# Kernel optimization log

Hardware: AMD Instinct MI355X
Metric: run time of the kernel (lower is better)

## Reference

```python
import jax, jax.numpy as jnp
import numpy as np

B, S, L, D = 128, 256, 200, 768
POS_VOCAB, POS_DIM = 60, 50
REDUC, HID, TAGS, POL = 400, 150, 5, 4


def setup_inputs() -> dict:
    key = jax.random.key(0)
    ks = jax.random.split(key, 12)
    bert_vectors = jax.random.normal(ks[0], (B, S, D), dtype=jnp.float32)
    # ragged subword spans: word j covers subwords [start_j, end_j] (inclusive), length 1..3,
    # skipping the [CLS] token at index 0. Clipped to S-1 (long sentences just truncate).
    rng = np.random.default_rng(0)
    lens = rng.integers(1, 4, size=(B, L))
    cum = np.cumsum(lens, axis=1)
    starts = 1 + cum - lens
    ends = cum
    starts = np.minimum(starts, S - 1)
    ends = np.minimum(ends, S - 1)
    ends = np.maximum(ends, starts)
    positions = jnp.asarray(np.stack([starts, ends], axis=-1), dtype=jnp.int32)
    postag = jax.random.randint(ks[1], (B, L), 1, POS_VOCAB).astype(jnp.int32)

    def lin(k, o, i):
        return jax.random.normal(k, (o, i), jnp.float32) / np.float32(np.sqrt(i))

    return dict(
        bert_vectors=bert_vectors,
        positions=positions,
        postag=postag,
        embed_table=jax.random.normal(ks[2], (POS_VOCAB, POS_DIM), jnp.float32) * 0.02,
        W_reduc=lin(ks[3], REDUC, D + POS_DIM), b_reduc=jnp.zeros((REDUC,), jnp.float32),
        W_ap=lin(ks[4], HID, REDUC), b_ap=jnp.zeros((HID,), jnp.float32),
        W_op=lin(ks[5], HID, REDUC), b_op=jnp.zeros((HID,), jnp.float32),
        W_ap2=lin(ks[6], HID, REDUC), b_ap2=jnp.zeros((HID,), jnp.float32),
        W_op2=lin(ks[7], HID, REDUC), b_op2=jnp.zeros((HID,), jnp.float32),
        W_aptag=lin(ks[8], TAGS, HID), b_aptag=jnp.zeros((TAGS,), jnp.float32),
        W_optag=lin(ks[9], TAGS, HID), b_optag=jnp.zeros((TAGS,), jnp.float32),
        W_bi=lin(ks[10], POL * HID, HID + 1),
    )


def _pool_subwords(vectors, positions):
    # variable-length mean pooling of subword vectors into word vectors
    # vectors: [B,S,D], positions: [B,L,2] -> [B,L,D]
    idx = jnp.arange(S)[None, None, :]                      # [1,1,S]
    p0 = positions[..., 0][..., None]                       # [B,L,1]
    p1 = positions[..., 1][..., None]
    m = ((idx >= p0) & (idx <= p1)).astype(vectors.dtype)   # [B,L,S]
    cnt = jnp.maximum(m.sum(-1, keepdims=True), 1.0)
    return jnp.einsum('bls,bsd->bld', m, vectors) / cnt


def reference(bert_vectors, positions, postag, embed_table,
              W_reduc, b_reduc, W_ap, b_ap, W_op, b_op,
              W_ap2, b_ap2, W_op2, b_op2,
              W_aptag, b_aptag, W_optag, b_optag, W_bi):
    word_vecs = _pool_subwords(bert_vectors, positions)                 # [B,L,D]
    pos_emb = embed_table[postag]                                       # [B,L,50]
    h = jnp.concatenate([pos_emb, word_vecs], axis=-1)                  # [B,L,D+50]
    reduc = jnp.einsum('blf,of->blo', h, W_reduc) + b_reduc             # [B,L,400]
    ap_rep = jax.nn.relu(jnp.einsum('blf,of->blo', reduc, W_ap) + b_ap)
    op_rep = jax.nn.relu(jnp.einsum('blf,of->blo', reduc, W_op) + b_op)
    ap_node = jax.nn.relu(jnp.einsum('blf,of->blo', reduc, W_ap2) + b_ap2)
    op_node = jax.nn.relu(jnp.einsum('blf,of->blo', reduc, W_op2) + b_op2)
    ap_out = jnp.einsum('blf,of->blo', ap_rep, W_aptag) + b_aptag       # [B,L,5]
    op_out = jnp.einsum('blf,of->blo', op_rep, W_optag) + b_optag       # [B,L,5]
    # Biaffine(150,150,POL,bias=(True,False))
    ones = jnp.ones((B, L, 1), ap_node.dtype)
    in1 = jnp.concatenate([ap_node, ones], axis=-1)                     # [B,L,151]
    affine = jnp.einsum('bli,oi->blo', in1, W_bi).reshape(B, L * POL, HID)
    tri = jnp.einsum('bkh,bmh->bkm', affine, op_node)                   # [B,L*POL,L]
    triplet_out = tri.transpose(0, 2, 1).reshape(B, L, L, POL)          # [B,L2,L1,POL]
    return (ap_out, op_out, triplet_out)
```

## Files before the change

kernel.cpp:

```cpp
#include <hip/hip_runtime.h>
#include <hip/hip_bf16.h>

#define Bsz 128
#define Ssz 256
#define Lsz 200
#define Dsz 768
#define POS_DIM 50
#define TAGS 5
#define NROW 25600
#define FIN 818
#define KH 832
#define KD 160
#define KW 416

typedef __attribute__((ext_vector_type(8))) short short8;
typedef __attribute__((ext_vector_type(4))) short short4v;
typedef __attribute__((ext_vector_type(4))) float floatx4;

__device__ __forceinline__ short f2bf(float v) {
    __hip_bfloat16 h = __float2bfloat16(v);
    short s; __builtin_memcpy(&s, &h, 2); return s;
}
__device__ __forceinline__ float bf2f(short s) {
    __hip_bfloat16 h; __builtin_memcpy(&h, &s, 2);
    return __bfloat162float(h);
}

__device__ __forceinline__ void gload16(const short* g, short* l) {
    __builtin_amdgcn_global_load_lds(
        (const __attribute__((address_space(1))) void*)g,
        (__attribute__((address_space(3))) void*)l, 16, 0, 0);
}

__global__ void prep_kernel(const float* __restrict__ W_reduc,
                            const float* __restrict__ W_ap, const float* __restrict__ W_op,
                            const float* __restrict__ W_ap2, const float* __restrict__ W_op2,
                            const float* __restrict__ W_bi,
                            const float* __restrict__ b_reduc,
                            const float* __restrict__ b_ap, const float* __restrict__ b_op,
                            const float* __restrict__ b_ap2, const float* __restrict__ b_op2,
                            short* __restrict__ Wh_bf, short* __restrict__ WrT_bf,
                            short* __restrict__ Wbi_bf,
                            float* __restrict__ b2, float* __restrict__ bbi_pad)
{
    int i = blockIdx.x * blockDim.x + threadIdx.x;
    if (i < 640 * KW) {
        int r = i / KW, c = i % KW;
        float v = 0.0f;
        if (r < 600 && c < 400) {
            const float* src = (r < 150) ? W_ap : (r < 300) ? W_op : (r < 450) ? W_ap2 : W_op2;
            v = src[(r % 150) * 400 + c];
        }
        Wh_bf[i] = f2bf(v);
    }
    if (i < 896 * KW) {
        int k = i / KW, c = i % KW;
        float v = 0.0f;
        if (c < 400) {
            int sc = -1;
            if (k < 768)      sc = POS_DIM + k;
            else if (k < 818) sc = k - 768;
            if (sc >= 0) v = W_reduc[c * FIN + sc];
        }
        WrT_bf[i] = f2bf(v);
    }
    if (i < 640 * KD) {
        int r = i / KD, c = i % KD;
        Wbi_bf[i] = (r < 600 && c < 150) ? f2bf(W_bi[r * 151 + c]) : (short)0;
    }
    if (i < 640) {
        float v = 0.0f;
        if (i < 600) {
            const float* bs = (i < 150) ? b_ap : (i < 300) ? b_op : (i < 450) ? b_ap2 : b_op2;
            v = bs[i % 150];
            const float* wsrc = (i < 150) ? W_ap : (i < 300) ? W_op : (i < 450) ? W_ap2 : W_op2;
            const float* wrow = wsrc + (i % 150) * 400;
            float d = 0.0f;
            for (int c = 0; c < 400; ++c) d += wrow[c] * b_reduc[c];
            v += d;
        }
        b2[i] = v;
        bbi_pad[i] = (i < 600) ? W_bi[i * 151 + 150] : 0.0f;
    }
}

__global__ __launch_bounds__(256) void pool_kernel(
    const float* __restrict__ bert,
    const int* __restrict__ positions,
    const int* __restrict__ postag,
    const float* __restrict__ embed,
    short* __restrict__ h_bf)
{
    int row = blockIdx.x;
    int b = row / Lsz;
    int st = positions[row * 2 + 0];
    int en = positions[row * 2 + 1];
    int tag = postag[row];
    int span = en - st + 1;
    float inv = 1.0f / (float)span;
    const float* base = bert + ((long)b * Ssz + st) * Dsz;
    short* hr = h_bf + (long)row * KH;

    int t = threadIdx.x;
    int c0 = t * 4;
    if (c0 >= KH) return;
    short4v o;
    if (c0 < 768) {
        float4 s = {0.f, 0.f, 0.f, 0.f};
        for (int i = 0; i < span; ++i) {
            float4 v = *(const float4*)(base + i * Dsz + c0);
            s.x += v.x; s.y += v.y; s.z += v.z; s.w += v.w;
        }
        o.x = f2bf(s.x * inv); o.y = f2bf(s.y * inv);
        o.z = f2bf(s.z * inv); o.w = f2bf(s.w * inv);
    } else {
        const float* e = embed + tag * POS_DIM;
#pragma unroll
        for (int j = 0; j < 4; ++j) {
            int c = c0 + j - 768;
            float v = (c < POS_DIM) ? e[c] : 0.0f;
            ((short*)&o)[j] = f2bf(v);
        }
    }
    *(short4v*)(hr + c0) = o;
}

__global__ __launch_bounds__(256) void gemm_mfma(
    const short* __restrict__ A, long long sAb, int lda,
    const short* __restrict__ Bt, long long sBb, int ldb,
    const float* __restrict__ bias,
    short* __restrict__ outB, float* __restrict__ outF, long long sCb, int ldc,
    int M, int Nv, int K, int mode)
{
    __shared__ __align__(16) short AB[16384];

    int bz = blockIdx.z;
    A += (long long)bz * sAb;
    Bt += (long long)bz * sBb;

    int bx = blockIdx.x, by = blockIdx.y;
    if (gridDim.z == 1) {
        int nwg = gridDim.x * gridDim.y;
        int orig = by * gridDim.x + bx;
        int q = nwg >> 3, r = nwg & 7;
        int xcd = orig & 7, idx = orig >> 3;
        int swz = (xcd < r ? xcd * (q + 1) : r * (q + 1) + (xcd - r) * q) + idx;
        bx = swz % gridDim.x;
        by = swz / gridDim.x;
    }

    int row0 = by * 128;
    int col0 = bx * 128;
    int tid = threadIdx.x;
    int lane = tid & 63;
    int wv = tid >> 6;
    int lm = lane & 15, lk = lane >> 4;
    int wr = (wv >> 1) * 64;
    int wc = (wv & 1) * 64;

    int c0 = tid, c1 = tid + 256;
    const short* gA0 = A + (long)(row0 + (c0 & 127)) * lda + (c0 >> 7) * 8;
    const short* gA1 = A + (long)(row0 + (c1 & 127)) * lda + (c1 >> 7) * 8;
    const short* gB0 = Bt + (long)(col0 + (c0 & 127)) * ldb + (c0 >> 7) * 8;
    const short* gB1 = Bt + (long)(col0 + (c1 & 127)) * ldb + (c1 >> 7) * 8;

    floatx4 acc[4][4];
#pragma unroll
    for (int i = 0; i < 4; ++i)
#pragma unroll
        for (int j = 0; j < 4; ++j)
            acc[i][j] = (floatx4){0.f, 0.f, 0.f, 0.f};

    auto stage = [&](int buf, int koff) {
        short* base = &AB[buf * 8192];
        gload16(gA0 + koff, base + c0 * 8);
        gload16(gA1 + koff, base + c1 * 8);
        gload16(gB0 + koff, base + 4096 + c0 * 8);
        gload16(gB1 + koff, base + 4096 + c1 * 8);
    };
    auto compute = [&](int buf) {
        const short* fa = &AB[buf * 8192 + (lk * 128 + wr + lm) * 8];
        const short* fb = &AB[buf * 8192 + 4096 + (lk * 128 + wc + lm) * 8];
        short8 a[4], b[4];
#pragma unroll
        for (int mt = 0; mt < 4; ++mt) a[mt] = *(const short8*)(fa + mt * 128);
#pragma unroll
        for (int nt = 0; nt < 4; ++nt) b[nt] = *(const short8*)(fb + nt * 128);
#pragma unroll
        for (int mt = 0; mt < 4; ++mt)
#pragma unroll
            for (int nt = 0; nt < 4; ++nt)
                acc[mt][nt] = __builtin_amdgcn_mfma_f32_16x16x32_bf16(
                    a[mt], b[nt], acc[mt][nt], 0, 0, 0);
    };

    int nt = K >> 5;
    stage(0, 0);
    __syncthreads();
    int cur = 0;
    for (int t = 0; t + 1 < nt; ++t) {
        stage(cur ^ 1, (t + 1) << 5);
        compute(cur);
        __syncthreads();
        cur ^= 1;
    }
    compute(cur);

#pragma unroll
    for (int mt = 0; mt < 4; ++mt) {
#pragma unroll
        for (int nt = 0; nt < 4; ++nt) {
#pragma unroll
            for (int r = 0; r < 4; ++r) {
                int gm = row0 + wr + mt * 16 + lk * 4 + r;
                int gn = col0 + wc + nt * 16 + lm;
                float v = acc[mt][nt][r];
                if (mode == 0 || mode == 4) {
                    if (gn < Nv)
                        outB[(long)gm * ldc + gn] = f2bf(mode == 0 ? v + bias[gn] : v);
                } else if (mode == 1) {
                    if (gn < 600) {
                        v = fmaxf(v + bias[gn], 0.0f);
                        outB[((long)(gn / 150) * NROW + gm) * KD + gn % 150] = f2bf(v);
                    } else if (gn < 640) {
                        int q = gn - 600;
                        outB[((long)(q / 10) * NROW + gm) * KD + 150 + q % 10] = 0;
                    }
                } else if (mode == 2) {
                    int bb = gm / 200, l = gm % 200;
                    if (gn < 600) {
                        v += bias[gn];
                        outB[((long)bb * 800 + l * 4 + gn / 150) * KD + gn % 150] = f2bf(v);
                    } else if (gn < 640) {
                        int q = gn - 600;
                        outB[((long)bb * 800 + l * 4 + q / 10) * KD + 150 + q % 10] = 0;
                    }
                } else {
                    if (gm < M && gn < Nv)
                        outF[(long long)bz * sCb + (long)gm * ldc + gn] = v;
                }
            }
        }
    }
}

__global__ __launch_bounds__(256) void gemm_mfma64(
    const short* __restrict__ A, int lda,
    const short* __restrict__ Bt, int ldb,
    const float* __restrict__ bias,
    short* __restrict__ outB, int K)
{
    __shared__ __align__(16) short AB[24576];

    int bx = blockIdx.x, by = blockIdx.y;
    {
        int nwg = gridDim.x * gridDim.y;
        int orig = by * gridDim.x + bx;
        int q = nwg >> 3, r = nwg & 7;
        int xcd = orig & 7, idx = orig >> 3;
        int swz = (xcd < r ? xcd * (q + 1) : r * (q + 1) + (xcd - r) * q) + idx;
        bx = swz % gridDim.x;
        by = swz / gridDim.x;
    }

    int row0 = by * 64;
    int col0 = bx * 128;
    int tid = threadIdx.x;
    int lane = tid & 63;
    int wv = tid >> 6;
    int lm = lane & 15, lk = lane >> 4;

    int a0 = tid, a1 = tid + 256;
    const short* gA0 = A + (long)(row0 + (a0 & 63)) * lda + (a0 >> 6) * 8;
    const short* gA1 = A + (long)(row0 + (a1 & 63)) * lda + (a1 >> 6) * 8;
    const short* gB[4];
    int bc[4];
#pragma unroll
    for (int i = 0; i < 4; ++i) {
        bc[i] = tid + i * 256;
        gB[i] = Bt + (long)(col0 + (bc[i] & 127)) * ldb + (bc[i] >> 7) * 8;
    }

    floatx4 acc[4][2];
#pragma unroll
    for (int i = 0; i < 4; ++i)
#pragma unroll
        for (int j = 0; j < 2; ++j)
            acc[i][j] = (floatx4){0.f, 0.f, 0.f, 0.f};

    auto stage = [&](int buf, int koff) {
        short* base = &AB[buf * 12288];
        gload16(gA0 + koff, base + a0 * 8);
        gload16(gA1 + koff, base + a1 * 8);
#pragma unroll
        for (int i = 0; i < 4; ++i)
            gload16(gB[i] + koff, base + 4096 + bc[i] * 8);
    };
    auto compute = [&](int buf) {
        const short* base = &AB[buf * 12288];
#pragma unroll
        for (int kk = 0; kk < 2; ++kk) {
            const short* fa = base + ((kk * 4 + lk) * 64 + lm) * 8;
            const short* fb = base + 4096 + ((kk * 4 + lk) * 128 + wv * 32 + lm) * 8;
            short8 a[4], b[2];
#pragma unroll
            for (int mt = 0; mt < 4; ++mt) a[mt] = *(const short8*)(fa + mt * 128);
#pragma unroll
            for (int nt = 0; nt < 2; ++nt) b[nt] = *(const short8*)(fb + nt * 128);
#pragma unroll
            for (int mt = 0; mt < 4; ++mt)
#pragma unroll
                for (int nt = 0; nt < 2; ++nt)
                    acc[mt][nt] = __builtin_amdgcn_mfma_f32_16x16x32_bf16(
                        a[mt], b[nt], acc[mt][nt], 0, 0, 0);
        }
    };

    int nt = K >> 6;
    stage(0, 0);
    __syncthreads();
    int cur = 0;
    for (int t = 0; t + 1 < nt; ++t) {
        stage(cur ^ 1, (t + 1) << 6);
        compute(cur);
        __syncthreads();
        cur ^= 1;
    }
    compute(cur);

#pragma unroll
    for (int mt = 0; mt < 4; ++mt) {
#pragma unroll
        for (int nt = 0; nt < 2; ++nt) {
#pragma unroll
            for (int r = 0; r < 4; ++r) {
                int gm = row0 + mt * 16 + lk * 4 + r;
                int gn = col0 + wv * 32 + nt * 16 + lm;
                float v = acc[mt][nt][r];
                if (gn < 600) {
                    v = fmaxf(v + bias[gn], 0.0f);
                    outB[((long)(gn / 150) * NROW + gm) * KD + gn % 150] = f2bf(v);
                } else if (gn < 640) {
                    int q = gn - 600;
                    outB[((long)(q / 10) * NROW + gm) * KD + 150 + q % 10] = 0;
                }
            }
        }
    }
}

__global__ __launch_bounds__(256) void tags_kernel(
    const short* __restrict__ hid4,
    const float* __restrict__ W_aptag, const float* __restrict__ b_aptag,
    const float* __restrict__ W_optag, const float* __restrict__ b_optag,
    float* __restrict__ out_ap, float* __restrict__ out_op)
{
    int wave = threadIdx.x / 64;
    int lane = threadIdx.x % 64;
    int row = blockIdx.x * 4 + wave;
    if (row >= NROW) return;

#pragma unroll
    for (int which = 0; which < 2; ++which) {
        const short* rep = hid4 + ((long)which * NROW + row) * KD;
        const float* W = which ? W_optag : W_aptag;
        const float* bb = which ? b_optag : b_aptag;
        float* out = which ? out_op : out_ap;
        float v0 = bf2f(rep[lane]);
        float v1 = bf2f(rep[64 + lane]);
        float v2 = (lane < 22) ? bf2f(rep[128 + lane]) : 0.0f;
#pragma unroll
        for (int t = 0; t < TAGS; ++t) {
            const float* w = W + t * 150;
            float p = v0 * w[lane] + v1 * w[64 + lane] +
                      ((lane < 22) ? v2 * w[128 + lane] : 0.0f);
#pragma unroll
            for (int off = 32; off > 0; off >>= 1) p += __shfl_down(p, off);
            if (lane == 0) out[row * TAGS + t] = p + bb[t];
        }
    }
}

extern "C" void kernel_launch(void* const* d_in, const int* in_sizes, int n_in,
                              void* d_out, int out_size, void* d_ws, size_t ws_size,
                              hipStream_t stream)
{
    const float* bert      = (const float*)d_in[0];
    const int*   positions = (const int*)d_in[1];
    const int*   postag    = (const int*)d_in[2];
    const float* embed     = (const float*)d_in[3];
    const float* W_reduc   = (const float*)d_in[4];
    const float* b_reduc   = (const float*)d_in[5];
    const float* W_ap      = (const float*)d_in[6];
    const float* b_ap      = (const float*)d_in[7];
    const float* W_op      = (const float*)d_in[8];
    const float* b_op      = (const float*)d_in[9];
    const float* W_ap2     = (const float*)d_in[10];
    const float* b_ap2     = (const float*)d_in[11];
    const float* W_op2     = (const float*)d_in[12];
    const float* b_op2     = (const float*)d_in[13];
    const float* W_aptag   = (const float*)d_in[14];
    const float* b_aptag   = (const float*)d_in[15];
    const float* W_optag   = (const float*)d_in[16];
    const float* b_optag   = (const float*)d_in[17];
    const float* W_bi      = (const float*)d_in[18];

    float* out = (float*)d_out;
    float* out_ap  = out;
    float* out_op  = out + NROW * TAGS;
    float* out_tri = out + 2 * NROW * TAGS;

    short* ws = (short*)d_ws;
    short* h_bf     = ws;
    short* affine   = h_bf;
    short* hid4     = h_bf + (long)NROW * KH;
    short* W2_bf    = hid4 + (long)4 * NROW * KD;
    short* Wh_bf    = W2_bf + 640 * KH;
    short* WrT_bf   = Wh_bf + 640 * KW;
    short* Wbi_bf   = WrT_bf + 896 * KW;
    float* b2       = (float*)(Wbi_bf + 640 * KD);
    float* bbi_pad  = b2 + 640;

    prep_kernel<<<(896 * KW + 255) / 256, 256, 0, stream>>>(
        W_reduc, W_ap, W_op, W_ap2, W_op2, W_bi,
        b_reduc, b_ap, b_op, b_ap2, b_op2,
        Wh_bf, WrT_bf, Wbi_bf, b2, bbi_pad);

    {
        dim3 g(7, 5, 1);
        gemm_mfma<<<g, 256, 0, stream>>>(Wh_bf, 0, KW, WrT_bf, 0, KW, nullptr,
                                         W2_bf, nullptr, 0, KH,
                                         640, KH, KW, 4);
    }

    pool_kernel<<<NROW, 256, 0, stream>>>(bert, positions, postag, embed, h_bf);

    {
        dim3 g(5, NROW / 64, 1);
        gemm_mfma64<<<g, 256, 0, stream>>>(h_bf, KH, W2_bf, KH, b2, hid4, KH);
    }
    tags_kernel<<<NROW / 4, 256, 0, stream>>>(hid4, W_aptag, b_aptag,
                                              W_optag, b_optag, out_ap, out_op);
    {
        dim3 g(5, NROW / 128, 1);
        gemm_mfma<<<g, 256, 0, stream>>>(hid4 + (long)2 * NROW * KD, 0, KD,
                                         Wbi_bf, 0, KD, bbi_pad,
                                         affine, nullptr, 0, 0,
                                         NROW, 600, KD, 2);
    }
    {
        dim3 g(7, 2, Bsz);
        gemm_mfma<<<g, 256, 0, stream>>>(hid4 + (long)3 * NROW * KD, (long long)200 * KD, KD,
                                         affine, (long long)800 * KD, KD, nullptr,
                                         nullptr, out_tri, (long long)200 * 800, 800,
                                         200, 800, KD, 3);
    }
}
```

Measured before the change: 451.7 us.

## Rewrite hidden-layer GEMM with 256x128 tiles and triple-buffered async pipeline

Replaces the 64x128-tile hidden projection GEMM with a 512-thread kernel using 256x128 tiles, 8 waves each covering 64x64, and a three-stage LDS ring buffer. Global loads for stage t+2 are interleaved between MFMA groups and gated by explicit vmcnt waits and raw barriers, with s_setprio raised around the MFMA bursts. The larger tile raises arithmetic intensity and the deeper pipeline hides load latency. In exchange it uses 144KB of LDS and more registers per wave, which limits occupancy, and the K loop is hardcoded to 13 steps. The unused mode 1 branch of the generic GEMM is also removed.

```diff
diff --git a/kernel.cpp b/kernel.cpp
--- a/kernel.cpp
+++ b/kernel.cpp
@@ -218,14 +218,6 @@
                 if (mode == 0 || mode == 4) {
                     if (gn < Nv)
                         outB[(long)gm * ldc + gn] = f2bf(mode == 0 ? v + bias[gn] : v);
-                } else if (mode == 1) {
-                    if (gn < 600) {
-                        v = fmaxf(v + bias[gn], 0.0f);
-                        outB[((long)(gn / 150) * NROW + gm) * KD + gn % 150] = f2bf(v);
-                    } else if (gn < 640) {
-                        int q = gn - 600;
-                        outB[((long)(q / 10) * NROW + gm) * KD + 150 + q % 10] = 0;
-                    }
                 } else if (mode == 2) {
                     int bb = gm / 200, l = gm % 200;
                     if (gn < 600) {
@@ -244,13 +236,13 @@
     }
 }
 
-__global__ __launch_bounds__(256) void gemm_mfma64(
-    const short* __restrict__ A, int lda,
-    const short* __restrict__ Bt, int ldb,
+__global__ __launch_bounds__(512, 2) void gemm_hid(
+    const short* __restrict__ A,
+    const short* __restrict__ Bt,
     const float* __restrict__ bias,
-    short* __restrict__ outB, int K)
-{
-    __shared__ __align__(16) short AB[24576];
+    short* __restrict__ outB)
+{
+    __shared__ __align__(16) short AB[73728];
 
     int bx = blockIdx.x, by = blockIdx.y;
     {
@@ -262,81 +254,126 @@
         bx = swz % gridDim.x;
         by = swz / gridDim.x;
     }
-
-    int row0 = by * 64;
+    int row0 = by * 256;
     int col0 = bx * 128;
     int tid = threadIdx.x;
     int lane = tid & 63;
     int wv = tid >> 6;
+    int wm = wv >> 1;
+    int wn = wv & 1;
     int lm = lane & 15, lk = lane >> 4;
 
-    int a0 = tid, a1 = tid + 256;
-    const short* gA0 = A + (long)(row0 + (a0 & 63)) * lda + (a0 >> 6) * 8;
-    const short* gA1 = A + (long)(row0 + (a1 & 63)) * lda + (a1 >> 6) * 8;
-    const short* gB[4];
-    int bc[4];
+    int cA[4], cB[2];
+    const short* gA[4]; const short* gB[2];
 #pragma unroll
     for (int i = 0; i < 4; ++i) {
-        bc[i] = tid + i * 256;
-        gB[i] = Bt + (long)(col0 + (bc[i] & 127)) * ldb + (bc[i] >> 7) * 8;
-    }
-
-    floatx4 acc[4][2];
+        cA[i] = tid + i * 512;
+        gA[i] = A + (long)(row0 + (cA[i] & 255)) * KH + (cA[i] >> 8) * 8;
+    }
+#pragma unroll
+    for (int j = 0; j < 2; ++j) {
+        cB[j] = tid + j * 512;
+        gB[j] = Bt + (long)(col0 + (cB[j] & 127)) * KH + (cB[j] >> 7) * 8;
+    }
+
+    floatx4 acc[4][4];
 #pragma unroll
     for (int i = 0; i < 4; ++i)
 #pragma unroll
-        for (int j = 0; j < 2; ++j)
+        for (int j = 0; j < 4; ++j)
             acc[i][j] = (floatx4){0.f, 0.f, 0.f, 0.f};
 
-    auto stage = [&](int buf, int koff) {
-        short* base = &AB[buf * 12288];
-        gload16(gA0 + koff, base + a0 * 8);
-        gload16(gA1 + koff, base + a1 * 8);
-#pragma unroll
-        for (int i = 0; i < 4; ++i)
-            gload16(gB[i] + koff, base + 4096 + bc[i] * 8);
-    };
-    auto compute = [&](int buf) {
-        const short* base = &AB[buf * 12288];
-#pragma unroll
-        for (int kk = 0; kk < 2; ++kk) {
-            const short* fa = base + ((kk * 4 + lk) * 64 + lm) * 8;
-            const short* fb = base + 4096 + ((kk * 4 + lk) * 128 + wv * 32 + lm) * 8;
-            short8 a[4], b[2];
-#pragma unroll
-            for (int mt = 0; mt < 4; ++mt) a[mt] = *(const short8*)(fa + mt * 128);
-#pragma unroll
-            for (int nt = 0; nt < 2; ++nt) b[nt] = *(const short8*)(fb + nt * 128);
-#pragma unroll
-            for (int mt = 0; mt < 4; ++mt)
-#pragma unroll
-                for (int nt = 0; nt < 2; ++nt)
-                    acc[mt][nt] = __builtin_amdgcn_mfma_f32_16x16x32_bf16(
-                        a[mt], b[nt], acc[mt][nt], 0, 0, 0);
-        }
-    };
-
-    int nt = K >> 6;
-    stage(0, 0);
-    __syncthreads();
-    int cur = 0;
-    for (int t = 0; t + 1 < nt; ++t) {
-        stage(cur ^ 1, (t + 1) << 6);
-        compute(cur);
-        __syncthreads();
-        cur ^= 1;
-    }
-    compute(cur);
-
-#pragma unroll
-    for (int mt = 0; mt < 4; ++mt) {
-#pragma unroll
-        for (int nt = 0; nt < 2; ++nt) {
+#pragma unroll
+    for (int i = 0; i < 4; ++i) gload16(gA[i], &AB[cA[i] * 8]);
+#pragma unroll
+    for (int j = 0; j < 2; ++j) gload16(gB[j], &AB[16384 + cB[j] * 8]);
+#pragma unroll
+    for (int i = 0; i < 4; ++i) gload16(gA[i] + 64, &AB[24576 + cA[i] * 8]);
+#pragma unroll
+    for (int j = 0; j < 2; ++j) gload16(gB[j] + 64, &AB[24576 + 16384 + cB[j] * 8]);
+
+#define NT 13
+#pragma unroll
+    for (int t = 0; t < NT; ++t) {
+        const int s = t % 3;
+        if (t < NT - 1) { asm volatile("s_waitcnt vmcnt(6)" ::: "memory"); }
+        else           { asm volatile("s_waitcnt vmcnt(0)" ::: "memory"); }
+        __builtin_amdgcn_sched_barrier(0);
+        __builtin_amdgcn_s_barrier();
+        __builtin_amdgcn_sched_barrier(0);
+
+        const short* ab = &AB[s * 24576] + ((lk * 256) + wm * 64 + lm) * 8;
+        const short* bb = &AB[s * 24576 + 16384] + ((lk * 128) + wn * 64 + lm) * 8;
+        const bool st = (t + 2) < NT;
+        const int s2 = (t + 2) % 3;
+        const int koff2 = (t + 2) * 64;
+        short* sbA = &AB[s2 * 24576];
+        short* sbB = &AB[s2 * 24576 + 16384];
+
+        short8 a[4][2], b[2][2];
+#pragma unroll
+        for (int m = 0; m < 4; ++m) {
+            a[m][0] = *(const short8*)(ab + m * 128);
+            a[m][1] = *(const short8*)(ab + 8192 + m * 128);
+        }
+        b[0][0] = *(const short8*)(bb);
+        b[0][1] = *(const short8*)(bb + 4096);
+
+        b[1][0] = *(const short8*)(bb + 128);
+        b[1][1] = *(const short8*)(bb + 4096 + 128);
+        if (st) { gload16(gA[0] + koff2, sbA + cA[0] * 8);
+                  gload16(gA[1] + koff2, sbA + cA[1] * 8); }
+        __builtin_amdgcn_s_setprio(1);
+#pragma unroll
+        for (int m = 0; m < 4; ++m) {
+            acc[m][0] = __builtin_amdgcn_mfma_f32_16x16x32_bf16(a[m][0], b[0][0], acc[m][0], 0, 0, 0);
+            acc[m][0] = __builtin_amdgcn_mfma_f32_16x16x32_bf16(a[m][1], b[0][1], acc[m][0], 0, 0, 0);
+        }
+        __builtin_amdgcn_s_setprio(0);
+
+        b[0][0] = *(const short8*)(bb + 256);
+        b[0][1] = *(const short8*)(bb + 4096 + 256);
+        if (st) { gload16(gA[2] + koff2, sbA + cA[2] * 8);
+                  gload16(gA[3] + koff2, sbA + cA[3] * 8); }
+        __builtin_amdgcn_s_setprio(1);
+#pragma unroll
+        for (int m = 0; m < 4; ++m) {
+            acc[m][1] = __builtin_amdgcn_mfma_f32_16x16x32_bf16(a[m][0], b[1][0], acc[m][1], 0, 0, 0);
+            acc[m][1] = __builtin_amdgcn_mfma_f32_16x16x32_bf16(a[m][1], b[1][1], acc[m][1], 0, 0, 0);
+        }
+        __builtin_amdgcn_s_setprio(0);
+
+        b[1][0] = *(const short8*)(bb + 384);
+        b[1][1] = *(const short8*)(bb + 4096 + 384);
+        if (st) { gload16(gB[0] + koff2, sbB + cB[0] * 8);
+                  gload16(gB[1] + koff2, sbB + cB[1] * 8); }
+        __builtin_amdgcn_s_setprio(1);
+#pragma unroll
+        for (int m = 0; m < 4; ++m) {
+            acc[m][2] = __builtin_amdgcn_mfma_f32_16x16x32_bf16(a[m][0], b[0][0], acc[m][2], 0, 0, 0);
+            acc[m][2] = __builtin_amdgcn_mfma_f32_16x16x32_bf16(a[m][1], b[0][1], acc[m][2], 0, 0, 0);
+        }
+        __builtin_amdgcn_s_setprio(0);
+
+        __builtin_amdgcn_s_setprio(1);
+#pragma unroll
+        for (int m = 0; m < 4; ++m) {
+            acc[m][3] = __builtin_amdgcn_mfma_f32_16x16x32_bf16(a[m][0], b[1][0], acc[m][3], 0, 0, 0);
+            acc[m][3] = __builtin_amdgcn_mfma_f32_16x16x32_bf16(a[m][1], b[1][1], acc[m][3], 0, 0, 0);
+        }
+        __builtin_amdgcn_s_setprio(0);
+    }
+#undef NT
+
+#pragma unroll
+    for (int m = 0; m < 4; ++m) {
+#pragma unroll
+        for (int n = 0; n < 4; ++n) {
 #pragma unroll
             for (int r = 0; r < 4; ++r) {
-                int gm = row0 + mt * 16 + lk * 4 + r;
-                int gn = col0 + wv * 32 + nt * 16 + lm;
-                float v = acc[mt][nt][r];
+                int gm = row0 + wm * 64 + m * 16 + lk * 4 + r;
+                int gn = col0 + wn * 64 + n * 16 + lm;
+                float v = acc[m][n][r];
                 if (gn < 600) {
                     v = fmaxf(v + bias[gn], 0.0f);
                     outB[((long)(gn / 150) * NROW + gm) * KD + gn % 150] = f2bf(v);
@@ -436,8 +473,8 @@
     pool_kernel<<<NROW, 256, 0, stream>>>(bert, positions, postag, embed, h_bf);
 
     {
-        dim3 g(5, NROW / 64, 1);
-        gemm_mfma64<<<g, 256, 0, stream>>>(h_bf, KH, W2_bf, KH, b2, hid4, KH);
+        dim3 g(5, NROW / 256, 1);
+        gemm_hid<<<g, 512, 0, stream>>>(h_bf, W2_bf, b2, hid4);
     }
     tags_kernel<<<NROW / 4, 256, 0, stream>>>(hid4, W_aptag, b_aptag,
                                               W_optag, b_optag, out_ap, out_op);
```

Result: faster. 426.9 us (-5.5%).
